# Kernel optimization log

Hardware: AMD Instinct MI355X
Metric: run time of the kernel (lower is better)

The kernel has to match this reference:

```python
import jax, jax.numpy as jnp
import numpy as np

# ControllerLayer hyperparams (match init_kwargs)
ALPHA = 0.01
TOP_K = 2
TEMPERATURE = 1.0  # temperature == 1.0 -> no division (use_temperature False)


def setup_inputs() -> dict:
    key = jax.random.key(0)
    k1, k2 = jax.random.split(key)
    B, H, C, D = 8, 32, 2048, 128  # batch, n_heads(=output_dim), seq_len, head_dim(=input_dim)
    x = jax.random.normal(k1, (B, H, C, D), dtype=jnp.float32)
    # router projection weight, torch nn.Linear(input_dim, output_dim, bias=False) -> W: (output_dim, input_dim)
    W = jax.random.normal(k2, (H, D), dtype=jnp.float32) * (1.0 / np.sqrt(D).astype(np.float32))
    return {"x": x, "W": W}


def reference(x, W):
    # x: (B, H, C, D) -- q reshaped per-head features; W: (O, D) with O == H
    B, H, C, D = x.shape
    O = W.shape[0]
    logits = jnp.einsum('bhcd,od->bhco', x, W)          # router logits
    probs = jax.nn.softmax(logits, axis=-1)             # (B, H, C, O)
    topk_probs, topk_idx = jax.lax.top_k(probs, TOP_K)  # (B, H, C, K)

    # torch.gather along dim=1 (head axis): sel[b,h,c,j,d] = x[b, topk_idx[b,h,c,j], c, d]
    xb = jnp.broadcast_to(x[:, :, :, None, :], (B, H, C, TOP_K, D))
    idx = jnp.broadcast_to(topk_idx[..., None], (B, H, C, TOP_K, D))
    sel = jnp.take_along_axis(xb, idx, axis=1)          # (B, H, C, K, D)

    # weighted sum over the k selected heads
    y = jnp.einsum('bhck,bhckd->bhcd', topk_probs, sel)

    # auxiliary load-balancing loss
    router_probs = probs.mean(axis=(0, 1, 2))                                   # (O,)
    counts = jnp.zeros((O,), jnp.float32).at[topk_idx.ravel()].add(1.0)         # bincount
    router_fraction = counts / counts.sum()
    aux_loss = ALPHA * O * jnp.sum(router_probs * router_fraction)
    return y, aux_loss
```

## Files before the change

### kernel.cpp

```cpp
#include <hip/hip_runtime.h>

#define NSLOT 256

typedef double dbl4 __attribute__((ext_vector_type(4)));
typedef float  f32x4 __attribute__((ext_vector_type(4)));

__global__ __launch_bounds__(256) void prep_kernel(const float* __restrict__ W,
                                                   double* __restrict__ wd,
                                                   float* __restrict__ ws) {
  int i = blockIdx.x * 256 + threadIdx.x;
  ws[i] = 0.0f;
  if (i < 4096) {
    int d4 = i >> 7;
    int o  = (i >> 2) & 31;
    int k  = i & 3;
    wd[i] = (double)W[(o << 7) + (d4 << 2) + k];
  }
}

__global__ __launch_bounds__(512, 6) void moe_router_kernel(
    const float* __restrict__ x, const double* __restrict__ wd,
    float* __restrict__ y, float* __restrict__ ws) {
  __shared__ float  Xs[64 * 128];
  __shared__ double m1s[8][64];
  __shared__ double m2s[8][64];
  __shared__ int    jps[8][64];
  __shared__ float  sumS[8][64];

  const int tid = threadIdx.x;
  const int l   = tid & 63;
  const int wu  = __builtin_amdgcn_readfirstlane(tid >> 6);
  const int bc  = blockIdx.x;
  const int b   = bc >> 10;
  const int c0  = (bc & 1023) << 1;

  const float* xb = x + ((size_t)b * 32 * 2048 + c0) * 128;

  {
    auto ldsX = (__attribute__((address_space(3))) char*)Xs;
    #pragma unroll
    for (int rep = 0; rep < 4; ++rep) {
      int i   = (rep << 9) + tid;
      int row = i >> 5;
      int p   = i & 31;
      int h   = row & 31, t = row >> 5;
      int d4  = p ^ (row & 31);
      const float* src = xb + ((size_t)h * 2048 + t) * 128 + (d4 << 2);
      __builtin_amdgcn_global_load_lds(
          (const __attribute__((address_space(1))) void*)src,
          (__attribute__((address_space(3))) void*)(ldsX + (size_t)i * 16),
          16, 0, 0);
    }
  }
  __syncthreads();

  double a0 = 0.0, a1 = 0.0, a2 = 0.0, a3 = 0.0;
  const dbl4* __restrict__ wv4 = reinterpret_cast<const dbl4*>(wd);
  const int rsw  = l & 31;
  const int base = l << 7;
  float4 xv = *reinterpret_cast<const float4*>(&Xs[base + (rsw << 2)]);
  #pragma unroll 4
  for (int d4 = 0; d4 < 32; ++d4) {
    float4 xn = *reinterpret_cast<const float4*>(
        &Xs[base + ((((d4 + 1) & 31) ^ rsw) << 2)]);
    const dbl4* wc = wv4 + (d4 << 5) + (wu << 2);
    dbl4 w0 = wc[0], w1 = wc[1], w2 = wc[2], w3 = wc[3];
    double x0 = (double)xv.x, x1 = (double)xv.y, x2 = (double)xv.z, x3 = (double)xv.w;
    a0 = fma(x0, w0[0], a0); a0 = fma(x1, w0[1], a0);
    a0 = fma(x2, w0[2], a0); a0 = fma(x3, w0[3], a0);
    a1 = fma(x0, w1[0], a1); a1 = fma(x1, w1[1], a1);
    a1 = fma(x2, w1[2], a1); a1 = fma(x3, w1[3], a1);
    a2 = fma(x0, w2[0], a2); a2 = fma(x1, w2[1], a2);
    a2 = fma(x2, w2[2], a2); a2 = fma(x3, w2[3], a2);
    a3 = fma(x0, w3[0], a3); a3 = fma(x1, w3[1], a3);
    a3 = fma(x2, w3[2], a3); a3 = fma(x3, w3[3], a3);
    xv = xn;
  }

  double acc[4] = {a0, a1, a2, a3};
  double m1 = acc[0], m2 = -1.0e300;
  int    j1 = 0, j2 = 0;
  #pragma unroll
  for (int j = 1; j < 4; ++j) {
    double v = acc[j];
    if (v > m1)      { m2 = m1; j2 = j1; m1 = v; j1 = j; }
    else if (v > m2) { m2 = v; j2 = j; }
  }
  float e[4];
  float sloc = 0.0f;
  #pragma unroll
  for (int j = 0; j < 4; ++j) { e[j] = __expf((float)(acc[j] - m1)); sloc += e[j]; }

  m1s[wu][l]  = m1;
  m2s[wu][l]  = m2;
  jps[wu][l]  = (j1 + (wu << 2)) | ((j2 + (wu << 2)) << 8);
  sumS[wu][l] = sloc;
  __syncthreads();

  double M = -1.0e300, g2 = -1.0e300;
  int g1i = 0, g2i = 0;
  #pragma unroll
  for (int w = 0; w < 8; ++w) {
    double a  = m1s[w][l];
    double bb = m2s[w][l];
    int    jp = jps[w][l];
    if (a > M)       { g2 = M; g2i = g1i; M = a; g1i = jp & 255; }
    else if (a > g2) { g2 = a; g2i = jp & 255; }
    if (bb > g2)     { g2 = bb; g2i = (jp >> 8) & 255; }
  }
  float S = 0.0f;
  #pragma unroll
  for (int w = 0; w < 8; ++w)
    S += sumS[w][l] * __expf((float)(m1s[w][l] - M));
  const float invS = 1.0f / S;
  const float p1 = invS;
  const float p2 = __expf((float)(g2 - M)) * invS;
  const int   jpack = g1i | (g2i << 8);

  {
    const float f = __expf((float)(m1 - M)) * invS;
    float ps[4];
    #pragma unroll
    for (int j = 0; j < 4; ++j) ps[j] = e[j] * f;
    #pragma unroll
    for (int m = 1; m < 64; m <<= 1) {
      #pragma unroll
      for (int j = 0; j < 4; ++j) ps[j] += __shfl_xor(ps[j], m, 64);
    }
    const int slot = (bc & (NSLOT - 1)) << 5;
    if (l == 0) {
      #pragma unroll
      for (int j = 0; j < 4; ++j) atomicAdd(&ws[slot + (wu << 2) + j], ps[j]);
    }
    if (wu == 0) {
      float cnt = 0.0f;
      #pragma unroll
      for (int o = 0; o < 32; ++o) {
        float c = (float)(__popcll(__ballot(g1i == o)) + __popcll(__ballot(g2i == o)));
        if (l == o) cnt = c;
      }
      if (l < 32) atomicAdd(&ws[8192 + slot + l], cnt);
    }
  }

  float* yb = y + ((size_t)b * 32 * 2048 + c0) * 128;
  #pragma unroll
  for (int rep = 0; rep < 4; ++rep) {
    int i   = (rep << 9) + tid;
    int row = i >> 5;
    int d4  = i & 31;
    float q1 = __shfl(p1, row, 64);
    float q2 = __shfl(p2, row, 64);
    int   jp = __shfl(jpack, row, 64);
    int i1 = jp & 255, i2 = (jp >> 8) & 255;
    int t = row >> 5, h = row & 31;
    const float4 A  = *reinterpret_cast<const float4*>(
        &Xs[(((t << 5) + i1) << 7) + ((d4 ^ i1) << 2)]);
    const float4 Bv = *reinterpret_cast<const float4*>(
        &Xs[(((t << 5) + i2) << 7) + ((d4 ^ i2) << 2)]);
    f32x4 o4;
    o4.x = q1 * A.x + q2 * Bv.x;
    o4.y = q1 * A.y + q2 * Bv.y;
    o4.z = q1 * A.z + q2 * Bv.z;
    o4.w = q1 * A.w + q2 * Bv.w;
    __builtin_nontemporal_store(o4,
        reinterpret_cast<f32x4*>(yb + ((size_t)h * 2048 + t) * 128 + (d4 << 2)));
  }
}

__global__ __launch_bounds__(256) void finalize_kernel(const float* __restrict__ ws,
                                                       float* __restrict__ out_aux) {
  __shared__ double redP[8][32];
  __shared__ double redC[8][32];
  const int o = threadIdx.x & 31;
  const int g = threadIdx.x >> 5;
  double sp = 0.0, sc = 0.0;
  for (int s = g; s < NSLOT; s += 8) {
    sp += (double)ws[s * 32 + o];
    sc += (double)ws[8192 + s * 32 + o];
  }
  redP[g][o] = sp;
  redC[g][o] = sc;
  __syncthreads();
  if (threadIdx.x == 0) {
    double aux = 0.0;
    const double nrows  = 524288.0;
    const double ntotal = 1048576.0;
    for (int oo = 0; oo < 32; ++oo) {
      double tp = 0.0, tc = 0.0;
      for (int gg = 0; gg < 8; ++gg) { tp += redP[gg][oo]; tc += redC[gg][oo]; }
      aux += (tp / nrows) * (tc / ntotal);
    }
    out_aux[0] = (float)(0.01 * 32.0 * aux);
  }
}

extern "C" void kernel_launch(void* const* d_in, const int* in_sizes, int n_in,
                              void* d_out, int out_size, void* d_ws, size_t ws_size,
                              hipStream_t stream) {
  const float* x = (const float*)d_in[0];
  const float* W = (const float*)d_in[1];
  float*  y  = (float*)d_out;
  float*  ws = (float*)d_ws;
  double* wd = (double*)((char*)d_ws + 65536);

  prep_kernel<<<64, 256, 0, stream>>>(W, wd, ws);
  moe_router_kernel<<<8192, 512, 0, stream>>>(x, wd, y, ws);
  finalize_kernel<<<1, 256, 0, stream>>>(ws, y + (size_t)8 * 32 * 2048 * 128);
}
```

Measured before the change: 175.8 us.

## Compute router logits with FP64 MFMA and per-row softmax from LDS

Replaces the per-lane scalar FP64 FMA dot products with the 16x16x4 FP64 MFMA instruction. Each wave computes one 16x16 tile of the 64x32 logit matrix, and W is pre-laid out in prep so it can be loaded as the MFMA B operand. Logits are scattered to an LDS matrix, using an MFMA trick to compute output indices. Each lane then does a full 32-way top-2 and softmax on its own row, which replaces the cross-wave partial merge. The intent is to cut FP64 ALU cost on the matrix unit. In exchange every wave now repeats the 32-wide softmax scan, and the LDS row stride of 33 doubles may cause bank conflicts.

```diff
diff --git a/kernel.cpp b/kernel.cpp
--- a/kernel.cpp
+++ b/kernel.cpp
@@ -2,34 +2,34 @@
 
 #define NSLOT 256
 
-typedef double dbl4 __attribute__((ext_vector_type(4)));
+typedef double dbl4x __attribute__((ext_vector_type(4)));
 typedef float  f32x4 __attribute__((ext_vector_type(4)));
 
 __global__ __launch_bounds__(256) void prep_kernel(const float* __restrict__ W,
-                                                   double* __restrict__ wd,
+                                                   double* __restrict__ wd2,
                                                    float* __restrict__ ws) {
   int i = blockIdx.x * 256 + threadIdx.x;
   ws[i] = 0.0f;
   if (i < 4096) {
-    int d4 = i >> 7;
-    int o  = (i >> 2) & 31;
-    int k  = i & 3;
-    wd[i] = (double)W[(o << 7) + (d4 << 2) + k];
+    int k = i >> 5;
+    int o = i & 31;
+    wd2[i] = (double)W[(o << 7) + k];
   }
 }
 
 __global__ __launch_bounds__(512, 6) void moe_router_kernel(
-    const float* __restrict__ x, const double* __restrict__ wd,
+    const float* __restrict__ x, const double* __restrict__ wd2,
     float* __restrict__ y, float* __restrict__ ws) {
   __shared__ float  Xs[64 * 128];
-  __shared__ double m1s[8][64];
-  __shared__ double m2s[8][64];
-  __shared__ int    jps[8][64];
-  __shared__ float  sumS[8][64];
+  __shared__ double Ls[64 * 33];
 
   const int tid = threadIdx.x;
   const int l   = tid & 63;
   const int wu  = __builtin_amdgcn_readfirstlane(tid >> 6);
+  const int mtile = wu >> 1;
+  const int ntile = wu & 1;
+  const int c   = l & 15;
+  const int q   = l >> 4;
   const int bc  = blockIdx.x;
   const int b   = bc >> 10;
   const int c0  = (bc & 1023) << 1;
@@ -54,74 +54,55 @@
   }
   __syncthreads();
 
-  double a0 = 0.0, a1 = 0.0, a2 = 0.0, a3 = 0.0;
-  const dbl4* __restrict__ wv4 = reinterpret_cast<const dbl4*>(wd);
-  const int rsw  = l & 31;
-  const int base = l << 7;
-  float4 xv = *reinterpret_cast<const float4*>(&Xs[base + (rsw << 2)]);
-  #pragma unroll 4
-  for (int d4 = 0; d4 < 32; ++d4) {
-    float4 xn = *reinterpret_cast<const float4*>(
-        &Xs[base + ((((d4 + 1) & 31) ^ rsw) << 2)]);
-    const dbl4* wc = wv4 + (d4 << 5) + (wu << 2);
-    dbl4 w0 = wc[0], w1 = wc[1], w2 = wc[2], w3 = wc[3];
-    double x0 = (double)xv.x, x1 = (double)xv.y, x2 = (double)xv.z, x3 = (double)xv.w;
-    a0 = fma(x0, w0[0], a0); a0 = fma(x1, w0[1], a0);
-    a0 = fma(x2, w0[2], a0); a0 = fma(x3, w0[3], a0);
-    a1 = fma(x0, w1[0], a1); a1 = fma(x1, w1[1], a1);
-    a1 = fma(x2, w1[2], a1); a1 = fma(x3, w1[3], a1);
-    a2 = fma(x0, w2[0], a2); a2 = fma(x1, w2[1], a2);
-    a2 = fma(x2, w2[2], a2); a2 = fma(x3, w2[3], a2);
-    a3 = fma(x0, w3[0], a3); a3 = fma(x1, w3[1], a3);
-    a3 = fma(x2, w3[2], a3); a3 = fma(x3, w3[3], a3);
-    xv = xn;
+  const int rowA = (mtile << 4) + c;
+  const int rsw  = rowA & 31;
+  const int xbase = rowA << 7;
+  const double* bp = wd2 + (q << 5) + (ntile << 4) + c;
+  dbl4x acc = {0.0, 0.0, 0.0, 0.0};
+  #pragma unroll 8
+  for (int t = 0; t < 32; ++t) {
+    double a = (double)Xs[xbase + ((t ^ rsw) << 2) + q];
+    double bv = bp[t << 7];
+    acc = __builtin_amdgcn_mfma_f64_16x16x4f64(a, bv, acc, 0, 0, 0);
   }
 
-  double acc[4] = {a0, a1, a2, a3};
-  double m1 = acc[0], m2 = -1.0e300;
+  {
+    double a1 = (q == 0) ? (double)(33 * c) : 0.0;
+    double b1 = (q == 0) ? 1.0 : 0.0;
+    double b2 = (q == 0) ? (double)c : 0.0;
+    dbl4x ecc = {0.0, 0.0, 0.0, 0.0};
+    ecc = __builtin_amdgcn_mfma_f64_16x16x4f64(a1, b1, ecc, 0, 0, 0);
+    ecc = __builtin_amdgcn_mfma_f64_16x16x4f64(b1, b2, ecc, 0, 0, 0);
+    double* lbase = &Ls[((mtile << 4) * 33) + (ntile << 4)];
+    lbase[(int)ecc[0]] = acc[0];
+    lbase[(int)ecc[1]] = acc[1];
+    lbase[(int)ecc[2]] = acc[2];
+    lbase[(int)ecc[3]] = acc[3];
+  }
+  __syncthreads();
+
+  const double* lrow = &Ls[l * 33];
+  double m1 = -1.0e300, m2 = -1.0e300;
   int    j1 = 0, j2 = 0;
   #pragma unroll
-  for (int j = 1; j < 4; ++j) {
-    double v = acc[j];
-    if (v > m1)      { m2 = m1; j2 = j1; m1 = v; j1 = j; }
-    else if (v > m2) { m2 = v; j2 = j; }
-  }
-  float e[4];
-  float sloc = 0.0f;
-  #pragma unroll
-  for (int j = 0; j < 4; ++j) { e[j] = __expf((float)(acc[j] - m1)); sloc += e[j]; }
-
-  m1s[wu][l]  = m1;
-  m2s[wu][l]  = m2;
-  jps[wu][l]  = (j1 + (wu << 2)) | ((j2 + (wu << 2)) << 8);
-  sumS[wu][l] = sloc;
-  __syncthreads();
-
-  double M = -1.0e300, g2 = -1.0e300;
-  int g1i = 0, g2i = 0;
-  #pragma unroll
-  for (int w = 0; w < 8; ++w) {
-    double a  = m1s[w][l];
-    double bb = m2s[w][l];
-    int    jp = jps[w][l];
-    if (a > M)       { g2 = M; g2i = g1i; M = a; g1i = jp & 255; }
-    else if (a > g2) { g2 = a; g2i = jp & 255; }
-    if (bb > g2)     { g2 = bb; g2i = (jp >> 8) & 255; }
+  for (int o = 0; o < 32; ++o) {
+    double lv = lrow[o];
+    if (lv > m1)      { m2 = m1; j2 = j1; m1 = lv; j1 = o; }
+    else if (lv > m2) { m2 = lv; j2 = o; }
   }
   float S = 0.0f;
   #pragma unroll
-  for (int w = 0; w < 8; ++w)
-    S += sumS[w][l] * __expf((float)(m1s[w][l] - M));
+  for (int o = 0; o < 32; ++o) S += __expf((float)(lrow[o] - m1));
   const float invS = 1.0f / S;
   const float p1 = invS;
-  const float p2 = __expf((float)(g2 - M)) * invS;
-  const int   jpack = g1i | (g2i << 8);
+  const float p2 = __expf((float)(m2 - m1)) * invS;
+  const int   jpack = j1 | (j2 << 8);
 
   {
-    const float f = __expf((float)(m1 - M)) * invS;
     float ps[4];
     #pragma unroll
-    for (int j = 0; j < 4; ++j) ps[j] = e[j] * f;
+    for (int j = 0; j < 4; ++j)
+      ps[j] = __expf((float)(lrow[(wu << 2) + j] - m1)) * invS;
     #pragma unroll
     for (int m = 1; m < 64; m <<= 1) {
       #pragma unroll
@@ -136,8 +117,8 @@
       float cnt = 0.0f;
       #pragma unroll
       for (int o = 0; o < 32; ++o) {
-        float c = (float)(__popcll(__ballot(g1i == o)) + __popcll(__ballot(g2i == o)));
-        if (l == o) cnt = c;
+        float cc = (float)(__popcll(__ballot(j1 == o)) + __popcll(__ballot(j2 == o)));
+        if (l == o) cnt = cc;
       }
       if (l < 32) atomicAdd(&ws[8192 + slot + l], cnt);
     }
@@ -200,11 +181,11 @@
                               hipStream_t stream) {
   const float* x = (const float*)d_in[0];
   const float* W = (const float*)d_in[1];
-  float*  y  = (float*)d_out;
-  float*  ws = (float*)d_ws;
-  double* wd = (double*)((char*)d_ws + 65536);
+  float*  y   = (float*)d_out;
+  float*  ws  = (float*)d_ws;
+  double* wd2 = (double*)((char*)d_ws + 65536);
 
-  prep_kernel<<<64, 256, 0, stream>>>(W, wd, ws);
-  moe_router_kernel<<<8192, 512, 0, stream>>>(x, wd, y, ws);
+  prep_kernel<<<64, 256, 0, stream>>>(W, wd2, ws);
+  moe_router_kernel<<<8192, 512, 0, stream>>>(x, wd2, y, ws);
   finalize_kernel<<<1, 256, 0, stream>>>(ws, y + (size_t)8 * 32 * 2048 * 128);
 }
```

After: 189.1 us. +7.6%, slower.
